# Optimization experiments

Measured on AMD Instinct MI355X. Metric: run time of the kernel, lower is better.

The kernel has to match this reference:

```python
import jax, jax.numpy as jnp
import numpy as np
from jax import lax


def _lin_weights(in_size, out_size):
    # torch F.interpolate(mode='bilinear', align_corners=False) source indices
    scale = in_size / out_size
    src = (jnp.arange(out_size, dtype=jnp.float32) + 0.5) * scale - 0.5
    src = jnp.maximum(src, 0.0)
    i0 = jnp.minimum(jnp.floor(src).astype(jnp.int32), in_size - 1)
    i1 = jnp.minimum(i0 + 1, in_size - 1)
    w = src - i0.astype(jnp.float32)
    return i0, i1, w


def bilinear_resize(x, out_h, out_w):
    # x: (..., H, W) -> (..., out_h, out_w), separable bilinear
    H, W = x.shape[-2], x.shape[-1]
    i0, i1, wh = _lin_weights(H, out_h)
    j0, j1, ww = _lin_weights(W, out_w)
    x = x[..., i0, :] * (1.0 - wh)[:, None] + x[..., i1, :] * wh[:, None]
    x = x[..., :, j0] * (1.0 - ww) + x[..., :, j1] * ww
    return x


def setup_inputs() -> dict:
    key = jax.random.key(0)
    ks = jax.random.split(key, 16)
    b, H, W = 16, 56, 56
    n = H * W
    dim, heads, dh, agent_num = 512, 8, 64, 49
    ID = heads * dh  # inner_dim == dim
    s = 0.02
    return {
        'x': jax.random.normal(ks[0], (b, n, dim), jnp.float32),
        'H': H, 'W': W,
        'q_w': s * jax.random.normal(ks[1], (dim, ID), jnp.float32),
        'q_b': s * jax.random.normal(ks[2], (ID,), jnp.float32),
        'kv_w': s * jax.random.normal(ks[3], (dim, 2 * ID), jnp.float32),
        'kv_b': s * jax.random.normal(ks[4], (2 * ID,), jnp.float32),
        'proj_w': s * jax.random.normal(ks[5], (ID, dim), jnp.float32),
        'proj_b': s * jax.random.normal(ks[6], (dim,), jnp.float32),
        'dwc_w': s * jax.random.normal(ks[7], (ID, 1, 3, 3), jnp.float32),
        'dwc_b': s * jax.random.normal(ks[8], (ID,), jnp.float32),
        'an_bias': s * jax.random.normal(ks[9], (heads, agent_num, 7, 7), jnp.float32),
        'na_bias': s * jax.random.normal(ks[10], (heads, agent_num, 7, 7), jnp.float32),
        'ah_bias': s * jax.random.normal(ks[11], (1, heads, agent_num, H, 1), jnp.float32),
        'aw_bias': s * jax.random.normal(ks[12], (1, heads, agent_num, 1, W), jnp.float32),
        'ha_bias': s * jax.random.normal(ks[13], (1, heads, H, 1, agent_num), jnp.float32),
        'wa_bias': s * jax.random.normal(ks[14], (1, heads, 1, W, agent_num), jnp.float32),
    }


def reference(x, H, W, q_w, q_b, kv_w, kv_b, proj_w, proj_b, dwc_w, dwc_b,
              an_bias, na_bias, ah_bias, aw_bias, ha_bias, wa_bias):
    b, n, c = x.shape
    heads, agent_num = an_bias.shape[0], an_bias.shape[1]
    ID = q_w.shape[1]
    dh = ID // heads
    scale = dh ** -0.5
    pool = int(round(agent_num ** 0.5))  # 7

    q = x @ q_w + q_b                      # (b, n, ID)
    kv = x @ kv_w + kv_b                   # (b, n, 2*ID)  (sr_ratio == 1)
    k, v = kv[..., :ID], kv[..., ID:]

    # adaptive avg pool of q on the (H, W) grid -> agent tokens (b, agent_num, ID)
    qi = q.reshape(b, pool, H // pool, pool, W // pool, ID)
    agent = qi.mean(axis=(2, 4)).reshape(b, agent_num, ID)

    qh = q.reshape(b, n, heads, dh).transpose(0, 2, 1, 3)          # (b,h,n,d)
    kh = k.reshape(b, n, heads, dh).transpose(0, 2, 1, 3)
    vh = v.reshape(b, n, heads, dh).transpose(0, 2, 1, 3)
    ah = agent.reshape(b, agent_num, heads, dh).transpose(0, 2, 1, 3)  # (b,h,a,d)

    # stage 1: agent tokens attend to k/v, with interpolated + factored position bias
    pb1 = bilinear_resize(an_bias, H, W).reshape(1, heads, agent_num, n)
    pb2 = (ah_bias + aw_bias).reshape(1, heads, agent_num, n)
    s1 = jnp.einsum('bhad,bhnd->bhan', ah * scale, kh) + pb1 + pb2
    agent_attn = jax.nn.softmax(s1, axis=-1)                        # (b,h,a,n)
    agent_v = jnp.einsum('bhan,bhnd->bhad', agent_attn, vh)         # (b,h,a,d)

    # stage 2: queries attend to agent tokens
    ab1 = bilinear_resize(na_bias, H, W).reshape(1, heads, agent_num, n).transpose(0, 1, 3, 2)
    ab2 = (ha_bias + wa_bias).reshape(1, heads, n, agent_num)
    s2 = jnp.einsum('bhnd,bhad->bhna', qh * scale, ah) + ab1 + ab2
    q_attn = jax.nn.softmax(s2, axis=-1)                            # (b,h,n,a)
    out = jnp.einsum('bhna,bhad->bhnd', q_attn, agent_v)
    out = out.transpose(0, 2, 1, 3).reshape(b, n, ID)

    # depthwise 3x3 conv over v as spatial residual
    v_img = v.reshape(b, H, W, ID).transpose(0, 3, 1, 2)            # (b,ID,H,W)
    dwc = lax.conv_general_dilated(v_img, dwc_w, (1, 1), 'SAME',
                                   feature_group_count=ID,
                                   dimension_numbers=('NCHW', 'OIHW', 'NCHW'))
    dwc = dwc + dwc_b[None, :, None, None]
    out = out + dwc.transpose(0, 2, 3, 1).reshape(b, n, ID)

    return out @ proj_w + proj_b
```

## Files before the change

### kernel.cpp

```cpp
#include <hip/hip_runtime.h>
#include <hip/hip_bf16.h>

#define DEV __device__ __forceinline__

typedef __attribute__((ext_vector_type(4))) float f32x4;
typedef __attribute__((ext_vector_type(8))) short bf8_t;
typedef __attribute__((ext_vector_type(4))) unsigned int u32x4;

static constexpr float QSCALE = 0.125f;

DEV float bflo(unsigned int w){ union{unsigned int i; float f;} x; x.i = w << 16; return x.f; }
DEV float bfhi(unsigned int w){ union{unsigned int i; float f;} x; x.i = w & 0xffff0000u; return x.f; }
DEV float bf2f(unsigned short u){ union{unsigned int i; float f;} x; x.i = ((unsigned int)u) << 16; return x.f; }
DEV unsigned short f2bf(float f){
  union{float f; unsigned int i;} x; x.f = f;
  unsigned int i = x.i;
  i += 0x7fffu + ((i >> 16) & 1u);
  return (unsigned short)(i >> 16);
}
DEV unsigned int pack2(float a, float b){ return (unsigned int)f2bf(a) | ((unsigned int)f2bf(b) << 16); }

DEV void mfma_acc(f32x4& c, const bf8_t& a, const bf8_t& b){
  asm volatile("v_mfma_f32_16x16x32_bf16 %0, %1, %2, %0" : "+v"(c) : "v"(a), "v"(b));
}

DEV void cp16(unsigned short* l, const unsigned short* g){
  __builtin_amdgcn_global_load_lds(
      (const __attribute__((address_space(1))) unsigned int*)(const void*)g,
      (__attribute__((address_space(3))) unsigned int*)(void*)l, 16, 0, 0);
}

DEV float wred_max(float v){
  #pragma unroll
  for (int m = 1; m < 64; m <<= 1) v = fmaxf(v, __shfl_xor(v, m));
  return v;
}
DEV float wred_sum(float v){
  #pragma unroll
  for (int m = 1; m < 64; m <<= 1) v += __shfl_xor(v, m);
  return v;
}

__global__ void k_prep(const float* __restrict__ qw, const float* __restrict__ kvw,
                       const float* __restrict__ pw, const float* __restrict__ qb,
                       const float* __restrict__ kvb,
                       unsigned short* __restrict__ wqkvt, unsigned short* __restrict__ wprojt,
                       float* __restrict__ qkvbias){
  const int i0 = blockIdx.x * blockDim.x + threadIdx.x;
  const int stride = gridDim.x * blockDim.x;
  for (int idx = i0; idx < 1536*512; idx += stride){
    int n = idx >> 9, k = idx & 511;
    float v = (n < 512) ? qw[k*512 + n] : kvw[k*1024 + (n - 512)];
    wqkvt[idx] = f2bf(v);
  }
  for (int idx = i0; idx < 512*512; idx += stride){
    int n = idx >> 9, k = idx & 511;
    wprojt[idx] = f2bf(pw[k*512 + n]);
  }
  for (int idx = i0; idx < 1536; idx += stride)
    qkvbias[idx] = (idx < 512) ? qb[idx] : kvb[idx - 512];
}

__global__ void k_cvt_x(const float* __restrict__ x, unsigned short* __restrict__ xb){
  const long total8 = (long)50176*512/8;
  for (long i = (long)blockIdx.x*blockDim.x + threadIdx.x; i < total8; i += (long)gridDim.x*blockDim.x){
    const float4* p = (const float4*)(x + i*8);
    float4 a = p[0], b = p[1];
    u32x4 o;
    o.x = pack2(a.x, a.y); o.y = pack2(a.z, a.w);
    o.z = pack2(b.x, b.y); o.w = pack2(b.z, b.w);
    *(u32x4*)(xb + i*8) = o;
  }
}

template<bool OUT_BF>
__global__ __launch_bounds__(256) void k_gemm(const unsigned short* __restrict__ A,
    const unsigned short* __restrict__ Bt, const float* __restrict__ bias,
    void* __restrict__ Cp, const int N, const int nxb){
  __shared__ unsigned short Al[128][64];
  __shared__ unsigned short Bl[128][64];
  const int tid = threadIdx.x, lane = tid & 63, w = tid >> 6;
  const int bid = blockIdx.x;
  const int cxd = bid & 7, kk = bid >> 3;
  const int yi = kk / nxb, xb = kk - yi*nxb;
  const int m0 = (cxd + 8*yi) * 128, n0 = xb * 128;
  const int wr = (w >> 1) * 64, wc = (w & 1) * 64;
  const int fr = lane & 15, kg = lane >> 4;

  const int lr = lane >> 3, slog = (lane & 7) ^ lr;
  const unsigned short* gA = A  + (size_t)(m0 + w*32 + lr)*512 + slog*8;
  const unsigned short* gB = Bt + (size_t)(n0 + w*32 + lr)*512 + slog*8;

  f32x4 acc[4][4] = {};
  for (int kt = 0; kt < 8; ++kt){
    const int k0 = kt * 64;
    __syncthreads();
    #pragma unroll
    for (int cch = 0; cch < 4; ++cch){
      cp16(&Al[w*32 + cch*8][0], gA + (size_t)cch*8*512 + k0);
      cp16(&Bl[w*32 + cch*8][0], gB + (size_t)cch*8*512 + k0);
    }
    __syncthreads();
    bf8_t afl[4], afh[4];
    #pragma unroll
    for (int i = 0; i < 4; ++i){
      const int row = wr + i*16 + fr;
      const int sl = (kg ^ (row & 7)) * 8;
      afl[i] = *(const bf8_t*)&Al[row][sl];
      afh[i] = *(const bf8_t*)&Al[row][sl ^ 32];
    }
    #pragma unroll
    for (int j = 0; j < 4; ++j){
      const int row = wc + j*16 + fr;
      const int sl = (kg ^ (row & 7)) * 8;
      bf8_t bfl = *(const bf8_t*)&Bl[row][sl];
      bf8_t bfh = *(const bf8_t*)&Bl[row][sl ^ 32];
      #pragma unroll
      for (int i = 0; i < 4; ++i){
        mfma_acc(acc[i][j], afl[i], bfl);
        mfma_acc(acc[i][j], afh[i], bfh);
      }
    }
  }
  const int rb = kg * 4;
  #pragma unroll
  for (int j = 0; j < 4; ++j){
    const int col = n0 + wc + j*16 + fr;
    const float bs = bias[col];
    #pragma unroll
    for (int i = 0; i < 4; ++i){
      #pragma unroll
      for (int r = 0; r < 4; ++r){
        const int row = m0 + wr + i*16 + rb + r;
        float v = acc[i][j][r] + bs;
        if (OUT_BF) ((unsigned short*)Cp)[(size_t)row*N + col] = f2bf(v);
        else        ((float*)Cp)[(size_t)row*N + col] = v;
      }
    }
  }
}

__global__ void k_pool(const unsigned short* __restrict__ qkv, float* __restrict__ agent){
  const int b = blockIdx.x / 49, a = blockIdx.x % 49;
  const int p1 = a / 7, p2 = a % 7;
  for (int c = threadIdx.x; c < 512; c += 256){
    float s = 0.f;
    for (int r = 0; r < 8; ++r)
      for (int cc = 0; cc < 8; ++cc){
        int pix = (p1*8 + r)*56 + p2*8 + cc;
        s += bf2f(qkv[((size_t)b*3136 + pix)*1536 + c]);
      }
    agent[((size_t)b*49 + a)*512 + c] = s * (1.0f/64.0f);
  }
}

DEV void lin_w(int o, int& i0, int& i1, float& w){
  float src = (o + 0.5f)*0.125f - 0.5f;
  src = fmaxf(src, 0.f);
  int f = (int)floorf(src);
  i0 = min(f, 6); i1 = min(i0 + 1, 6); w = src - (float)i0;
}

__global__ void k_bias(const float* __restrict__ an, const float* __restrict__ ahb,
                       const float* __restrict__ awb,
                       const float* __restrict__ na, const float* __restrict__ hab,
                       const float* __restrict__ wab,
                       float* __restrict__ pbs, float* __restrict__ absumT){
  const int tot = 8*49*3136;
  for (int idx = blockIdx.x*blockDim.x + threadIdx.x; idx < tot; idx += gridDim.x*blockDim.x){
    int n = idx % 3136, ha = idx / 3136;
    int a = ha % 49, h = ha / 49;
    int y = n / 56, x = n % 56;
    int iy0, iy1, ix0, ix1; float wy, wx;
    lin_w(y, iy0, iy1, wy); lin_w(x, ix0, ix1, wx);
    {
      const float* t = an + (size_t)ha*49;
      float v0 = t[iy0*7+ix0]*(1.f-wy) + t[iy1*7+ix0]*wy;
      float v1 = t[iy0*7+ix1]*(1.f-wy) + t[iy1*7+ix1]*wy;
      float v = v0*(1.f-wx) + v1*wx;
      pbs[idx] = v + ahb[ha*56 + y] + awb[ha*56 + x];
    }
    {
      const float* t = na + (size_t)ha*49;
      float v0 = t[iy0*7+ix0]*(1.f-wy) + t[iy1*7+ix0]*wy;
      float v1 = t[iy0*7+ix1]*(1.f-wy) + t[iy1*7+ix1]*wy;
      float v = v0*(1.f-wx) + v1*wx;
      absumT[idx] = v + hab[(h*56+y)*49 + a] + wab[(h*56+x)*49 + a];
    }
  }
}

__global__ __launch_bounds__(256) void k_attn1(const unsigned short* __restrict__ qkv,
    const float* __restrict__ agent, const float* __restrict__ pbs,
    float* __restrict__ pacc, float* __restrict__ pml){
  const int bi = blockIdx.x;
  const int sp = bi % 7, h = (bi/7) & 7, b = bi / 56;
  const int tid = threadIdx.x, lane = tid & 63, w = tid >> 6;
  const int c = lane & 15, kg = lane >> 4;

  __shared__ unsigned short ag[64][72];
  __shared__ unsigned short Kl[64][72];
  __shared__ unsigned short Vt[64][72];
  __shared__ unsigned short Pl[4][16][72];

  for (int it = tid; it < 64*8; it += 256){
    int a = it >> 3, o = it & 7;
    u32x4 wv = {0,0,0,0};
    if (a < 49){
      const float* p = agent + ((size_t)b*49 + a)*512 + h*64 + o*8;
      f32x4 lo = *(const f32x4*)p, hi = *(const f32x4*)(p+4);
      wv.x = pack2(lo.x*QSCALE, lo.y*QSCALE);
      wv.y = pack2(lo.z*QSCALE, lo.w*QSCALE);
      wv.z = pack2(hi.x*QSCALE, hi.y*QSCALE);
      wv.w = pack2(hi.z*QSCALE, hi.w*QSCALE);
    }
    *(u32x4*)&ag[a][o*8] = wv;
  }
  __syncthreads();
  bf8_t agf[2];
  agf[0] = *(const bf8_t*)&ag[w*16 + c][kg*8];
  agf[1] = *(const bf8_t*)&ag[w*16 + c][kg*8 + 32];

  const int aw = w*16 + c;
  const int amin = aw < 49 ? aw : 48;
  const bool areal = aw < 49;
  const float* pbrow = pbs + ((size_t)(h*49 + amin))*3136 + sp*448;

  float m_ = -1e30f, l_ = 0.f;
  f32x4 acc[4] = {};

  for (int t = 0; t < 7; ++t){
    const int gn0 = sp*448 + t*64;
    f32x4 pb4[4];
    #pragma unroll
    for (int i = 0; i < 4; ++i)
      pb4[i] = *(const f32x4*)(pbrow + t*64 + 16*i + 4*kg);

    __syncthreads();
    #pragma unroll
    for (int ii = 0; ii < 2; ++ii){
      int it = tid + ii*256;
      int pix = it >> 3, o = it & 7;
      const unsigned short* kp = qkv + ((size_t)b*3136 + gn0 + pix)*1536 + 512 + h*64 + o*8;
      *(u32x4*)&Kl[pix][o*8] = *(const u32x4*)kp;
    }
    #pragma unroll
    for (int ii = 0; ii < 2; ++ii){
      int it = tid + ii*256;
      int pix = it & 63, o = it >> 6;
      const unsigned short* vp = qkv + ((size_t)b*3136 + gn0 + pix)*1536 + 1024 + h*64 + o*8;
      u32x4 vv = *(const u32x4*)vp;
      unsigned int vals[4] = {vv.x, vv.y, vv.z, vv.w};
      #pragma unroll
      for (int q = 0; q < 4; ++q){
        Vt[o*8 + 2*q][pix]     = (unsigned short)(vals[q] & 0xffffu);
        Vt[o*8 + 2*q + 1][pix] = (unsigned short)(vals[q] >> 16);
      }
    }
    __syncthreads();

    f32x4 sa[4] = {};
    #pragma unroll
    for (int i = 0; i < 4; ++i){
      bf8_t kf0 = *(const bf8_t*)&Kl[i*16 + c][kg*8];
      bf8_t kf1 = *(const bf8_t*)&Kl[i*16 + c][kg*8 + 32];
      mfma_acc(sa[i], kf0, agf[0]);
      mfma_acc(sa[i], kf1, agf[1]);
    }

    float s16[4][4]; float mx = -1e30f;
    #pragma unroll
    for (int i = 0; i < 4; ++i)
      #pragma unroll
      for (int r = 0; r < 4; ++r){
        float sv = areal ? (sa[i][r] + pb4[i][r]) : -1e30f;
        s16[i][r] = sv; mx = fmaxf(mx, sv);
      }
    mx = fmaxf(mx, __shfl_xor(mx, 16));
    mx = fmaxf(mx, __shfl_xor(mx, 32));
    float mn = fmaxf(m_, mx);
    float al = __expf(m_ - mn);
    float rs = 0.f;
    #pragma unroll
    for (int i = 0; i < 4; ++i)
      #pragma unroll
      for (int r = 0; r < 4; ++r){
        float p = __expf(s16[i][r] - mn);
        s16[i][r] = p; rs += p;
      }
    rs += __shfl_xor(rs, 16);
    rs += __shfl_xor(rs, 32);
    m_ = mn; l_ = l_*al + rs;

    #pragma unroll
    for (int i = 0; i < 4; ++i){
      uint2 pw;
      pw.x = pack2(s16[i][0], s16[i][1]);
      pw.y = pack2(s16[i][2], s16[i][3]);
      *(uint2*)&Pl[w][c][16*i + 4*kg] = pw;
    }

    float al_s[4];
    #pragma unroll
    for (int r = 0; r < 4; ++r) al_s[r] = __shfl(al, 4*kg + r);
    #pragma unroll
    for (int j = 0; j < 4; ++j)
      #pragma unroll
      for (int r = 0; r < 4; ++r) acc[j][r] *= al_s[r];

    bf8_t pf0 = *(const bf8_t*)&Pl[w][c][kg*8];
    bf8_t pf1 = *(const bf8_t*)&Pl[w][c][kg*8 + 32];
    #pragma unroll
    for (int j = 0; j < 4; ++j){
      bf8_t vf0 = *(const bf8_t*)&Vt[j*16 + c][kg*8];
      bf8_t vf1 = *(const bf8_t*)&Vt[j*16 + c][kg*8 + 32];
      mfma_acc(acc[j], pf0, vf0);
      mfma_acc(acc[j], pf1, vf1);
    }
  }

  const int base = ((b*8 + h)*7 + sp)*49;
  #pragma unroll
  for (int r = 0; r < 4; ++r){
    const int a = w*16 + 4*kg + r;
    if (a < 49){
      float* dst = pacc + (size_t)(base + a)*64 + c;
      #pragma unroll
      for (int j = 0; j < 4; ++j) dst[16*j] = acc[j][r];
    }
  }
  if (kg == 0 && areal){
    pml[(base + aw)*2]     = m_;
    pml[(base + aw)*2 + 1] = l_;
  }
}

__global__ void k_merge(const float* __restrict__ pacc, const float* __restrict__ pml,
                        float* __restrict__ agentv){
  const int gw = blockIdx.x*4 + (threadIdx.x >> 6);
  const int lane = threadIdx.x & 63;
  if (gw >= 16*8*49) return;
  const int a = gw % 49, bh = gw / 49;
  float ms[7], ls[7], M = -1e30f;
  #pragma unroll
  for (int s = 0; s < 7; ++s){
    int base = (bh*7 + s)*49 + a;
    ms[s] = pml[base*2]; ls[s] = pml[base*2 + 1];
    M = fmaxf(M, ms[s]);
  }
  float L = 0.f, o = 0.f;
  #pragma unroll
  for (int s = 0; s < 7; ++s){
    float e = __expf(ms[s] - M);
    L += ls[s]*e;
    o += pacc[(size_t)((bh*7 + s)*49 + a)*64 + lane]*e;
  }
  agentv[(size_t)(bh*49 + a)*64 + lane] = o / L;
}

__global__ __launch_bounds__(256) void k_attn2(const unsigned short* __restrict__ qkv,
    const float* __restrict__ agent, const float* __restrict__ agentv,
    const float* __restrict__ absumT, unsigned short* __restrict__ outb){
  const int blk = blockIdx.x;
  const int bh = blk / 13, tloc = blk % 13;
  const int b = bh >> 3, h = bh & 7;
  const int tid = threadIdx.x, lane = tid & 63, w = tid >> 6;
  const int c = lane & 15, kg = lane >> 4;

  __shared__ unsigned short ag[64][72];
  __shared__ unsigned short avT[64][72];
  __shared__ unsigned short Pl[4][16][72];

  for (int it = tid; it < 64*8; it += 256){
    int a = it >> 3, o = it & 7;
    u32x4 wv = {0,0,0,0};
    if (a < 49){
      const float* p = agent + ((size_t)b*49 + a)*512 + h*64 + o*8;
      f32x4 lo = *(const f32x4*)p, hi = *(const f32x4*)(p+4);
      wv.x = pack2(lo.x*QSCALE, lo.y*QSCALE);
      wv.y = pack2(lo.z*QSCALE, lo.w*QSCALE);
      wv.z = pack2(hi.x*QSCALE, hi.y*QSCALE);
      wv.w = pack2(hi.z*QSCALE, hi.w*QSCALE);
    }
    *(u32x4*)&ag[a][o*8] = wv;
  }
  for (int it = tid; it < 64*64; it += 256){
    int a = it >> 6, d = it & 63;
    avT[d][a] = (a < 49) ? f2bf(agentv[((size_t)bh*49 + a)*64 + d]) : (unsigned short)0;
  }
  __syncthreads();

  const int ti = tloc*4 + w;
  if (ti >= 49) return;
  const int pix0 = ti*64;

  bf8_t af[4][2];
  #pragma unroll
  for (int i = 0; i < 4; ++i){
    af[i][0] = *(const bf8_t*)&ag[i*16 + c][kg*8];
    af[i][1] = *(const bf8_t*)&ag[i*16 + c][kg*8 + 32];
  }

  for (int j = 0; j < 4; ++j){
    const int pix = pix0 + 16*j + c;
    const unsigned short* qp = qkv + ((size_t)b*3136 + pix)*1536 + h*64;
    bf8_t qf0 = *(const bf8_t*)(qp + kg*8);
    bf8_t qf1 = *(const bf8_t*)(qp + kg*8 + 32);
    f32x4 sa[4] = {};
    #pragma unroll
    for (int i = 0; i < 4; ++i){
      mfma_acc(sa[i], af[i][0], qf0);
      mfma_acc(sa[i], af[i][1], qf1);
    }
    float s16[4][4]; float mx = -1e30f;
    #pragma unroll
    for (int i = 0; i < 4; ++i){
      #pragma unroll
      for (int r = 0; r < 4; ++r){
        int a = 16*i + 4*kg + r;
        int am = a < 49 ? a : 48;
        float bias = absumT[((size_t)h*49 + am)*3136 + pix];
        float sv = (a < 49) ? (sa[i][r] + bias) : -1e30f;
        s16[i][r] = sv; mx = fmaxf(mx, sv);
      }
    }
    mx = fmaxf(mx, __shfl_xor(mx, 16));
    mx = fmaxf(mx, __shfl_xor(mx, 32));
    float rs = 0.f;
    #pragma unroll
    for (int i = 0; i < 4; ++i){
      #pragma unroll
      for (int r = 0; r < 4; ++r){
        float p = __expf(s16[i][r] - mx);
        s16[i][r] = p; rs += p;
      }
    }
    rs += __shfl_xor(rs, 16);
    rs += __shfl_xor(rs, 32);
    #pragma unroll
    for (int i = 0; i < 4; ++i){
      uint2 pw;
      pw.x = pack2(s16[i][0], s16[i][1]);
      pw.y = pack2(s16[i][2], s16[i][3]);
      *(uint2*)&Pl[w][c][16*i + 4*kg] = pw;
    }
    bf8_t pf0 = *(const bf8_t*)&Pl[w][c][kg*8];
    bf8_t pf1 = *(const bf8_t*)&Pl[w][c][kg*8 + 32];
    f32x4 acc[4] = {};
    #pragma unroll
    for (int jd = 0; jd < 4; ++jd){
      bf8_t vf0 = *(const bf8_t*)&avT[jd*16 + c][kg*8];
      bf8_t vf1 = *(const bf8_t*)&avT[jd*16 + c][kg*8 + 32];
      mfma_acc(acc[jd], pf0, vf0);
      mfma_acc(acc[jd], pf1, vf1);
    }
    float l_s[4];
    #pragma unroll
    for (int r = 0; r < 4; ++r) l_s[r] = __shfl(rs, 4*kg + r);
    #pragma unroll
    for (int r = 0; r < 4; ++r){
      const int prow = pix0 + 16*j + 4*kg + r;
      unsigned short* op = outb + ((size_t)b*3136 + prow)*512 + h*64;
      float inv = 1.0f / l_s[r];
      #pragma unroll
      for (int jd = 0; jd < 4; ++jd)
        op[jd*16 + c] = f2bf(acc[jd][r] * inv);
    }
  }
}

__global__ __launch_bounds__(256) void k_dwc(const unsigned short* __restrict__ qkv,
    const float* __restrict__ dwcw, const float* __restrict__ dwcb,
    unsigned short* __restrict__ outb){
  const int b = blockIdx.x / 56, y = blockIdx.x % 56;
  const int tid = threadIdx.x;
  const int cg = tid & 127, xh = tid >> 7;
  const int c0 = cg*4;
  float wv[9][4], bv[4];
  #pragma unroll
  for (int j = 0; j < 4; ++j){
    bv[j] = dwcb[c0 + j];
    #pragma unroll
    for (int t = 0; t < 9; ++t) wv[t][j] = dwcw[(c0 + j)*9 + t];
  }
  for (int xi = 0; xi < 28; ++xi){
    const int x = xh*28 + xi;
    float o[4] = {bv[0], bv[1], bv[2], bv[3]};
    #pragma unroll
    for (int ky = 0; ky < 3; ++ky){
      int ny = y + ky - 1;
      if (ny < 0 || ny >= 56) continue;
      #pragma unroll
      for (int kx = 0; kx < 3; ++kx){
        int nx = x + kx - 1;
        if (nx < 0 || nx >= 56) continue;
        const unsigned short* vp = qkv + ((size_t)b*3136 + ny*56 + nx)*1536 + 1024 + c0;
        unsigned int v01 = *(const unsigned int*)vp;
        unsigned int v23 = *((const unsigned int*)vp + 1);
        const int t = ky*3 + kx;
        o[0] += wv[t][0]*bflo(v01); o[1] += wv[t][1]*bfhi(v01);
        o[2] += wv[t][2]*bflo(v23); o[3] += wv[t][3]*bfhi(v23);
      }
    }
    unsigned short* op = outb + ((size_t)b*3136 + y*56 + x)*512 + c0;
    unsigned int a01 = *(unsigned int*)op;
    unsigned int a23 = *((unsigned int*)op + 1);
    o[0] += bflo(a01); o[1] += bfhi(a01);
    o[2] += bflo(a23); o[3] += bfhi(a23);
    *(unsigned int*)op       = pack2(o[0], o[1]);
    *((unsigned int*)op + 1) = pack2(o[2], o[3]);
  }
}

extern "C" void kernel_launch(void* const* d_in, const int* in_sizes, int n_in,
                              void* d_out, int out_size, void* d_ws, size_t ws_size,
                              hipStream_t stream){
  const float* x       = (const float*)d_in[0];
  const float* q_w     = (const float*)d_in[3];
  const float* q_b     = (const float*)d_in[4];
  const float* kv_w    = (const float*)d_in[5];
  const float* kv_b    = (const float*)d_in[6];
  const float* proj_w  = (const float*)d_in[7];
  const float* proj_b  = (const float*)d_in[8];
  const float* dwc_w   = (const float*)d_in[9];
  const float* dwc_b   = (const float*)d_in[10];
  const float* an_bias = (const float*)d_in[11];
  const float* na_bias = (const float*)d_in[12];
  const float* ah_bias = (const float*)d_in[13];
  const float* aw_bias = (const float*)d_in[14];
  const float* ha_bias = (const float*)d_in[15];
  const float* wa_bias = (const float*)d_in[16];

  char* ws = (char*)d_ws;
  size_t off = 0;
  auto alloc = [&](size_t bytes) -> void* {
    void* p = ws + off;
    off += (bytes + 255) & ~(size_t)255;
    return p;
  };
  unsigned short* xb     = (unsigned short*)alloc((size_t)50176*512*2);
  unsigned short* qkv    = (unsigned short*)alloc((size_t)50176*1536*2);
  unsigned short* wqkvt  = (unsigned short*)alloc((size_t)1536*512*2);
  unsigned short* wprojt = (unsigned short*)alloc((size_t)512*512*2);
  float* qkvb   = (float*)alloc((size_t)1536*4);
  float* agent  = (float*)alloc((size_t)16*49*512*4);
  float* agentv = (float*)alloc((size_t)16*8*49*64*4);
  float* pbs    = (float*)alloc((size_t)8*49*3136*4);
  float* absumT = (float*)alloc((size_t)8*49*3136*4);
  float* pacc   = (float*)alloc((size_t)16*8*8*49*64*4);
  float* pml    = (float*)alloc((size_t)16*8*8*49*2*4);
  unsigned short* outb = (unsigned short*)alloc((size_t)50176*512*2);
  if (off > ws_size) return;

  k_prep<<<512, 256, 0, stream>>>(q_w, kv_w, proj_w, q_b, kv_b, wqkvt, wprojt, qkvb);
  k_cvt_x<<<2048, 256, 0, stream>>>(x, xb);
  k_gemm<true><<<4704, 256, 0, stream>>>(xb, wqkvt, qkvb, qkv, 1536, 12);
  k_pool<<<784, 256, 0, stream>>>(qkv, agent);
  k_bias<<<1024, 256, 0, stream>>>(an_bias, ah_bias, aw_bias, na_bias, ha_bias, wa_bias, pbs, absumT);
  k_attn1<<<896, 256, 0, stream>>>(qkv, agent, pbs, pacc, pml);
  k_merge<<<1568, 256, 0, stream>>>(pacc, pml, agentv);
  k_attn2<<<1664, 256, 0, stream>>>(qkv, agent, agentv, absumT, outb);
  k_dwc<<<896, 256, 0, stream>>>(qkv, dwc_w, dwc_b, outb);
  k_gemm<false><<<1568, 256, 0, stream>>>(outb, wprojt, proj_b, d_out, 512, 4);
}
```

Baseline: 381.1 us.

## Restructure depthwise conv to one pixel per wavefront with 16-byte channel loads

The depthwise 3x3 conv kernel used to loop serially over 28 pixels per thread with 8-byte loads. Now each thread handles one pixel and 8 channels using 16-byte vector loads, and each 64-lane group covers a full 512-channel pixel. The grid grows from 896 to 12544 blocks, with a block index swizzle that spreads neighbouring pixels across blocks. This trades per-thread weight reuse (each thread now reloads 72 weights) for far more parallelism and wider memory transactions.

```diff
diff --git a/kernel.cpp b/kernel.cpp
--- a/kernel.cpp
+++ b/kernel.cpp
@@ -472,44 +472,58 @@
 __global__ __launch_bounds__(256) void k_dwc(const unsigned short* __restrict__ qkv,
     const float* __restrict__ dwcw, const float* __restrict__ dwcb,
     unsigned short* __restrict__ outb){
-  const int b = blockIdx.x / 56, y = blockIdx.x % 56;
   const int tid = threadIdx.x;
-  const int cg = tid & 127, xh = tid >> 7;
-  const int c0 = cg*4;
-  float wv[9][4], bv[4];
-  #pragma unroll
-  for (int j = 0; j < 4; ++j){
-    bv[j] = dwcb[c0 + j];
-    #pragma unroll
-    for (int t = 0; t < 9; ++t) wv[t][j] = dwcw[(c0 + j)*9 + t];
-  }
-  for (int xi = 0; xi < 28; ++xi){
-    const int x = xh*28 + xi;
-    float o[4] = {bv[0], bv[1], bv[2], bv[3]};
-    #pragma unroll
-    for (int ky = 0; ky < 3; ++ky){
-      int ny = y + ky - 1;
-      if (ny < 0 || ny >= 56) continue;
-      #pragma unroll
-      for (int kx = 0; kx < 3; ++kx){
-        int nx = x + kx - 1;
-        if (nx < 0 || nx >= 56) continue;
-        const unsigned short* vp = qkv + ((size_t)b*3136 + ny*56 + nx)*1536 + 1024 + c0;
-        unsigned int v01 = *(const unsigned int*)vp;
-        unsigned int v23 = *((const unsigned int*)vp + 1);
-        const int t = ky*3 + kx;
-        o[0] += wv[t][0]*bflo(v01); o[1] += wv[t][1]*bfhi(v01);
-        o[2] += wv[t][2]*bflo(v23); o[3] += wv[t][3]*bfhi(v23);
-      }
-    }
-    unsigned short* op = outb + ((size_t)b*3136 + y*56 + x)*512 + c0;
-    unsigned int a01 = *(unsigned int*)op;
-    unsigned int a23 = *((unsigned int*)op + 1);
-    o[0] += bflo(a01); o[1] += bfhi(a01);
-    o[2] += bflo(a23); o[3] += bfhi(a23);
-    *(unsigned int*)op       = pack2(o[0], o[1]);
-    *((unsigned int*)op + 1) = pack2(o[2], o[3]);
-  }
+  const int oct = tid & 63, pxl = tid >> 6;
+  const int bid = blockIdx.x;
+  const int gp4 = (bid & 7) * 1568 + (bid >> 3);
+  const int gp = gp4 * 4 + pxl;
+  const int b = gp / 3136, pix = gp - b*3136;
+  const int y = pix / 56, x = pix - y*56;
+  const int c0 = oct * 8;
+
+  f32x4 w4[18];
+  const f32x4* wp = (const f32x4*)(dwcw + c0*9);
+  #pragma unroll
+  for (int i = 0; i < 18; ++i) w4[i] = wp[i];
+  #define W(j,t) (w4[((j)*9+(t)) >> 2][((j)*9+(t)) & 3])
+
+  float o[8];
+  {
+    f32x4 b0 = *(const f32x4*)(dwcb + c0);
+    f32x4 b1 = *(const f32x4*)(dwcb + c0 + 4);
+    o[0]=b0.x; o[1]=b0.y; o[2]=b0.z; o[3]=b0.w;
+    o[4]=b1.x; o[5]=b1.y; o[6]=b1.z; o[7]=b1.w;
+  }
+
+  const unsigned short* vbase = qkv + (size_t)b*3136*1536 + 1024 + c0;
+  #pragma unroll
+  for (int ky = 0; ky < 3; ++ky){
+    const int ny = y + ky - 1;
+    if ((unsigned)ny >= 56u) continue;
+    #pragma unroll
+    for (int kx = 0; kx < 3; ++kx){
+      const int nx = x + kx - 1;
+      if ((unsigned)nx >= 56u) continue;
+      u32x4 vv = *(const u32x4*)(vbase + (size_t)(ny*56 + nx)*1536);
+      const int t = ky*3 + kx;
+      o[0] += W(0,t)*bflo(vv.x); o[1] += W(1,t)*bfhi(vv.x);
+      o[2] += W(2,t)*bflo(vv.y); o[3] += W(3,t)*bfhi(vv.y);
+      o[4] += W(4,t)*bflo(vv.z); o[5] += W(5,t)*bfhi(vv.z);
+      o[6] += W(6,t)*bflo(vv.w); o[7] += W(7,t)*bfhi(vv.w);
+    }
+  }
+  #undef W
+
+  unsigned short* op = outb + (size_t)gp*512 + c0;
+  u32x4 a = *(u32x4*)op;
+  o[0] += bflo(a.x); o[1] += bfhi(a.x);
+  o[2] += bflo(a.y); o[3] += bfhi(a.y);
+  o[4] += bflo(a.z); o[5] += bfhi(a.z);
+  o[6] += bflo(a.w); o[7] += bfhi(a.w);
+  u32x4 r;
+  r.x = pack2(o[0], o[1]); r.y = pack2(o[2], o[3]);
+  r.z = pack2(o[4], o[5]); r.w = pack2(o[6], o[7]);
+  *(u32x4*)op = r;
 }
 
 extern "C" void kernel_launch(void* const* d_in, const int* in_sizes, int n_in,
@@ -560,6 +574,6 @@
   k_attn1<<<896, 256, 0, stream>>>(qkv, agent, pbs, pacc, pml);
   k_merge<<<1568, 256, 0, stream>>>(pacc, pml, agentv);
   k_attn2<<<1664, 256, 0, stream>>>(qkv, agent, agentv, absumT, outb);
-  k_dwc<<<896, 256, 0, stream>>>(qkv, dwc_w, dwc_b, outb);
+  k_dwc<<<12544, 256, 0, stream>>>(qkv, dwc_w, dwc_b, outb);
   k_gemm<false><<<1568, 256, 0, stream>>>(outb, wprojt, proj_b, d_out, 512, 4);
 }
```

Result: faster. 360.5 us (-5.4%).
